# Kernel optimization log

Hardware: AMD Instinct MI355X
Metric: run time of the kernel (lower is better)

The kernel has to match this reference:

```python
import jax, jax.numpy as jnp
import numpy as np

LSTM_SIZE = 32
NUM_OPS = 64
NUM_EDGE = 128
TEMPERATURE = 5.0
TANH_CONST = 2.5


def _lstm_cell(x, h, c, W_ih, W_hh, b_ih, b_hh):
    # PyTorch gate order: i, f, g, o
    g = x @ W_ih.T + b_ih + h @ W_hh.T + b_hh  # [4*H]
    i, f, gg, o = jnp.split(g, 4)
    c2 = jax.nn.sigmoid(f) * c + jax.nn.sigmoid(i) * jnp.tanh(gg)
    h2 = jax.nn.sigmoid(o) * jnp.tanh(c2)
    return h2, c2


def setup_inputs() -> dict:
    key = jax.random.key(0)
    ks = jax.random.split(key, 12)
    H, G, O = LSTM_SIZE, 4 * LSTM_SIZE, NUM_OPS
    s = 0.1
    return {
        "input_vars": jax.random.uniform(ks[0], (1, 1, H), jnp.float32, -s, s),
        "W_ih0": jax.random.uniform(ks[1], (G, H), jnp.float32, -s, s),
        "W_hh0": jax.random.uniform(ks[2], (G, H), jnp.float32, -s, s),
        "b_ih0": jax.random.uniform(ks[3], (G,), jnp.float32, -s, s),
        "b_hh0": jax.random.uniform(ks[4], (G,), jnp.float32, -s, s),
        "W_ih1": jax.random.uniform(ks[5], (G, H), jnp.float32, -s, s),
        "W_hh1": jax.random.uniform(ks[6], (G, H), jnp.float32, -s, s),
        "b_ih1": jax.random.uniform(ks[7], (G,), jnp.float32, -s, s),
        "b_hh1": jax.random.uniform(ks[8], (G,), jnp.float32, -s, s),
        "embd": jax.random.uniform(ks[9], (O, H), jnp.float32, -s, s),
        "W_pred": jax.random.uniform(ks[10], (O, H), jnp.float32, -s, s),
        "b_pred": jax.random.uniform(ks[11], (O,), jnp.float32, -s, s),
        "num_edge": NUM_EDGE,
    }


def reference(input_vars, W_ih0, W_hh0, b_ih0, b_hh0,
              W_ih1, W_hh1, b_ih1, b_hh1,
              embd, W_pred, b_pred, num_edge):
    H = input_vars.shape[-1]
    x0 = input_vars.reshape(H)
    z = jnp.zeros((H,), input_vars.dtype)
    key0 = jax.random.key(42)

    def step(carry, _):
        key, x, h0, c0, h1, c1 = carry
        h0, c0 = _lstm_cell(x, h0, c0, W_ih0, W_hh0, b_ih0, b_hh0)
        h1, c1 = _lstm_cell(h0, h1, c1, W_ih1, W_hh1, b_ih1, b_hh1)
        logits = TANH_CONST * jnp.tanh((h1 @ W_pred.T + b_pred) / TEMPERATURE)
        key, sub = jax.random.split(key)
        idx = jax.random.categorical(sub, logits)
        logp = jax.nn.log_softmax(logits)
        lp = logp[idx]
        ent = -jnp.sum(jnp.exp(logp) * logp)
        x = embd[idx]
        return (key, x, h0, c0, h1, c1), (lp, ent, idx)

    _, (lps, ents, arch) = jax.lax.scan(step, (key0, x0, z, z, z, z), None, length=num_edge)
    return jnp.sum(lps), jnp.sum(ents), arch
```

## Files before the change

kernel.cpp:

```cpp
#include <hip/hip_runtime.h>
#include <stdint.h>

namespace {

typedef float v2f __attribute__((ext_vector_type(2)));
typedef int   v2i __attribute__((ext_vector_type(2)));

constexpr int H      = 32;
constexpr int NEDGE  = 128;
constexpr float TINY   = 1.1754943508222875e-38f;
constexpr float L2E    = 1.4426950408889634f;
constexpr float LN2    = 0.6931471805599453f;

__device__ __forceinline__ void tf_round(uint32_t& x0, uint32_t& x1, int r) {
  x0 += x1;
  x1 = (x1 << r) | (x1 >> (32 - r));
  x1 ^= x0;
}

__device__ __forceinline__ void tf2x32(uint32_t k0, uint32_t k1,
                                       uint32_t& x0, uint32_t& x1) {
  const uint32_t ks2 = k0 ^ k1 ^ 0x1BD11BDAu;
  x0 += k0; x1 += k1;
  tf_round(x0,x1,13); tf_round(x0,x1,15); tf_round(x0,x1,26); tf_round(x0,x1, 6);
  x0 += k1;  x1 += ks2 + 1u;
  tf_round(x0,x1,17); tf_round(x0,x1,29); tf_round(x0,x1,16); tf_round(x0,x1,24);
  x0 += ks2; x1 += k0 + 2u;
  tf_round(x0,x1,13); tf_round(x0,x1,15); tf_round(x0,x1,26); tf_round(x0,x1, 6);
  x0 += k0;  x1 += k1 + 3u;
  tf_round(x0,x1,17); tf_round(x0,x1,29); tf_round(x0,x1,16); tf_round(x0,x1,24);
  x0 += k1;  x1 += ks2 + 4u;
  tf_round(x0,x1,13); tf_round(x0,x1,15); tf_round(x0,x1,26); tf_round(x0,x1, 6);
  x0 += ks2; x1 += k0 + 5u;
}

__device__ __forceinline__ float fexp(float x) {
  return __builtin_amdgcn_exp2f(x * L2E);
}
__device__ __forceinline__ float flog(float x) {
  return __builtin_amdgcn_logf(x) * LN2;
}
__device__ __forceinline__ float fsigmoid(float x) {
  return __builtin_amdgcn_rcpf(1.0f + __builtin_amdgcn_exp2f(-x * L2E));
}
__device__ __forceinline__ float ftanh(float x) {
  const float ax = __builtin_fabsf(x);
  const float t  = __builtin_amdgcn_exp2f(ax * (-2.0f * L2E));
  const float r  = (1.0f - t) * __builtin_amdgcn_rcpf(1.0f + t);
  return __builtin_copysignf(r, x);
}

__device__ __forceinline__ float rdlane(float v, int i) {
  return __int_as_float(__builtin_amdgcn_readlane(__float_as_int(v), i));
}

template <int CTRL>
__device__ __forceinline__ float dppf(float v) {
  return __int_as_float(__builtin_amdgcn_update_dpp(
      __float_as_int(v), __float_as_int(v), CTRL, 0xF, 0xF, false));
}

__device__ __forceinline__ float wave_sum64(float v) {
  v += dppf<0xB1>(v);
  v += dppf<0x4E>(v);
  v += dppf<0x141>(v);
  v += dppf<0x140>(v);
  return (rdlane(v, 15) + rdlane(v, 31)) + (rdlane(v, 47) + rdlane(v, 63));
}

__device__ __forceinline__ float wave_max64(float v) {
  v = fmaxf(v, dppf<0xB1>(v));
  v = fmaxf(v, dppf<0x4E>(v));
  v = fmaxf(v, dppf<0x141>(v));
  v = fmaxf(v, dppf<0x140>(v));
  return fmaxf(fmaxf(rdlane(v, 15), rdlane(v, 31)),
               fmaxf(rdlane(v, 47), rdlane(v, 63)));
}

__device__ __forceinline__ v2f pkfma(v2f a, v2f b, v2f c) {
  return __builtin_elementwise_fma(a, b, c);
}

__device__ __forceinline__ v2f permswap_pair(float g) {
  const v2i r = __builtin_amdgcn_permlane32_swap(
      __float_as_int(g), __float_as_int(g), false, false);
  return v2f{__int_as_float(r.x), __int_as_float(r.y)};
}

__global__ __launch_bounds__(192, 1)
void ctrl_kernel(const float* __restrict__ input_vars,
                 const float* __restrict__ W_ih0, const float* __restrict__ W_hh0,
                 const float* __restrict__ b_ih0, const float* __restrict__ b_hh0,
                 const float* __restrict__ W_ih1, const float* __restrict__ W_hh1,
                 const float* __restrict__ b_ih1, const float* __restrict__ b_hh1,
                 const float* __restrict__ embd,
                 const float* __restrict__ W_pred, const float* __restrict__ b_pred,
                 float* __restrict__ out) {
  const int tid  = threadIdx.x;
  const int lane = tid & 63;
  const int wid  = tid >> 6;
  const int rB   = lane + 64;

  __shared__ float4 Wh[2][8][128];
  __shared__ __align__(16) float embd_lds[64 * H];
  __shared__ __align__(16) float h0buf[2][H];
  __shared__ __align__(16) float gumbuf[4][64];
  __shared__ __align__(16) float xbuf[2][H];
  __shared__ __align__(16) float arch_lds[NEDGE];

  if (wid < 2) {
#define STAGE(MAT, SRC)                                                    \
  _Pragma("unroll")                                                        \
  for (int j = 0; j < 8; ++j) {                                            \
    const int i = tid + 128 * j;                                           \
    const int k4 = i & 7, row = i >> 3;                                    \
    Wh[MAT][k4][row] = reinterpret_cast<const float4*>(SRC)[row * 8 + k4]; \
  }
    STAGE(0, W_hh0)
    STAGE(1, W_hh1)
#undef STAGE
#pragma unroll
    for (int j = 0; j < 4; ++j)
      reinterpret_cast<float4*>(embd_lds)[tid + 128 * j] =
          reinterpret_cast<const float4*>(embd)[tid + 128 * j];
    if (tid < 8)
      reinterpret_cast<float4*>(&xbuf[0][0])[tid] =
          reinterpret_cast<const float4*>(input_vars)[tid];
  }

  const float* WX = (wid == 1) ? W_ih1 : W_ih0;
  float4 wxA[8], wxB[8];
#pragma unroll
  for (int q = 0; q < 8; ++q) {
    wxA[q] = reinterpret_cast<const float4*>(WX + lane * H)[q];
    wxB[q] = reinterpret_cast<const float4*>(WX + rB * H)[q];
  }
  const float bsum0A = b_ih0[lane] + b_hh0[lane];
  const float bsum0B = b_ih0[rB]   + b_hh0[rB];
  const float bsum1A = b_ih1[lane] + b_hh1[lane];
  const float bsum1B = b_ih1[rB]   + b_hh1[rB];
  const float bp = b_pred[lane];
  float4 wp4[8];
#pragma unroll
  for (int q = 0; q < 8; ++q)
    wp4[q] = reinterpret_cast<const float4*>(W_pred + lane * H)[q];

  float c0 = 0.f, h0v = 0.f;
  float c1 = 0.f, h1v = 0.f;
  v2f hoA01={0.f,0.f}, hoA23={0.f,0.f}, hoB01={0.f,0.f}, hoB23={0.f,0.f};
  uint32_t k0 = 0u, k1 = 42u;
  uint32_t s0c = 0u, s1c = 0u;
  float lp_sum = 0.f, ent_sum = 0.f;
  float logit_prev = 0.f;
  int   idx_prev = 0;

  if (wid == 2) {
#pragma unroll 1
    for (int p = 0; p < 2; ++p) {
      uint32_t r0 = 0u, r1 = (uint32_t)(lane & 1);
      tf2x32(k0, k1, r0, r1);
      const uint32_t n0 = (uint32_t)__builtin_amdgcn_readlane((int)r0, 0);
      const uint32_t n1 = (uint32_t)__builtin_amdgcn_readlane((int)r1, 0);
      const uint32_t s0 = (uint32_t)__builtin_amdgcn_readlane((int)r0, 1);
      const uint32_t s1 = (uint32_t)__builtin_amdgcn_readlane((int)r1, 1);
      uint32_t x0 = 0u, x1 = (uint32_t)lane;
      tf2x32(s0, s1, x0, x1);
      const uint32_t bits = x0 ^ x1;
      k0 = n0; k1 = n1;
      float u = __uint_as_float(0x3f800000u | (bits >> 9)) - 1.0f;
      u = fmaxf(u + TINY, TINY);
      gumbuf[p][lane] = -flog(-flog(u));
    }
  }
  __syncthreads();

  for (int t = 0; t < NEDGE; ++t) {
    v2f rA01={0.f,0.f}, rA23={0.f,0.f}, rB01={0.f,0.f}, rB23={0.f,0.f};

    if (wid == 0) {
      v2f xA01={0.f,0.f}, xA23={0.f,0.f}, xB01={0.f,0.f}, xB23={0.f,0.f};
#pragma unroll
      for (int q = 0; q < 8; ++q) {
        const float4 x4 =
            *reinterpret_cast<const float4*>(&xbuf[t & 1][4 * q]);
        xA01 = pkfma(v2f{x4.x, x4.y}, v2f{wxA[q].x, wxA[q].y}, xA01);
        xA23 = pkfma(v2f{x4.z, x4.w}, v2f{wxA[q].z, wxA[q].w}, xA23);
        xB01 = pkfma(v2f{x4.x, x4.y}, v2f{wxB[q].x, wxB[q].y}, xB01);
        xB23 = pkfma(v2f{x4.z, x4.w}, v2f{wxB[q].z, wxB[q].w}, xB23);
      }
      const float gA = bsum0A + ((xA01.x + xA01.y) + (xA23.x + xA23.y))
                              + ((hoA01.x + hoA01.y) + (hoA23.x + hoA23.y));
      const float gB = bsum0B + ((xB01.x + xB01.y) + (xB23.x + xB23.y))
                              + ((hoB01.x + hoB01.y) + (hoB23.x + hoB23.y));
      const v2f gif = permswap_pair(gA);
      const v2f ggo = permswap_pair(gB);
      c0 = fsigmoid(gif.y) * c0 + fsigmoid(gif.x) * ftanh(ggo.x);
      h0v = fsigmoid(ggo.y) * ftanh(c0);
      h0buf[t & 1][lane & 31] = h0v;
    } else if (wid == 1) {
#pragma unroll
      for (int q = 0; q < 8; ++q) {
        const float4 wA = Wh[1][q][lane];
        const float4 wB = Wh[1][q][rB];
        const v2f h01 = {rdlane(h1v, 4*q+0), rdlane(h1v, 4*q+1)};
        const v2f h23 = {rdlane(h1v, 4*q+2), rdlane(h1v, 4*q+3)};
        rA01 = pkfma(h01, v2f{wA.x, wA.y}, rA01);
        rA23 = pkfma(h23, v2f{wA.z, wA.w}, rA23);
        rB01 = pkfma(h01, v2f{wB.x, wB.y}, rB01);
        rB23 = pkfma(h23, v2f{wB.z, wB.w}, rB23);
      }
      if (t > 0) {
        const float e  = fexp(logit_prev);
        const float E  = wave_sum64(e);
        const float ES = wave_sum64(e * logit_prev);
        const float lse = flog(E);
        const float li  = rdlane(logit_prev, idx_prev);
        lp_sum  += li - lse;
        ent_sum += lse - ES / E;
      }
    } else {
      uint32_t r0 = 0u, r1 = (uint32_t)(lane & 1);
      tf2x32(k0, k1, r0, r1);
      k0  = (uint32_t)__builtin_amdgcn_readlane((int)r0, 0);
      k1  = (uint32_t)__builtin_amdgcn_readlane((int)r1, 0);
      s0c = (uint32_t)__builtin_amdgcn_readlane((int)r0, 1);
      s1c = (uint32_t)__builtin_amdgcn_readlane((int)r1, 1);
    }
    __syncthreads();

    if (wid == 0) {
      hoA01 = v2f{0.f,0.f}; hoA23 = v2f{0.f,0.f};
      hoB01 = v2f{0.f,0.f}; hoB23 = v2f{0.f,0.f};
#pragma unroll
      for (int q = 0; q < 8; ++q) {
        const float4 wA = Wh[0][q][lane];
        const float4 wB = Wh[0][q][rB];
        const v2f h01 = {rdlane(h0v, 4*q+0), rdlane(h0v, 4*q+1)};
        const v2f h23 = {rdlane(h0v, 4*q+2), rdlane(h0v, 4*q+3)};
        hoA01 = pkfma(h01, v2f{wA.x, wA.y}, hoA01);
        hoA23 = pkfma(h23, v2f{wA.z, wA.w}, hoA23);
        hoB01 = pkfma(h01, v2f{wB.x, wB.y}, hoB01);
        hoB23 = pkfma(h23, v2f{wB.z, wB.w}, hoB23);
      }
    } else if (wid == 1) {
#pragma unroll
      for (int q = 0; q < 8; ++q) {
        const float4 h4 =
            *reinterpret_cast<const float4*>(&h0buf[t & 1][4 * q]);
        rA01 = pkfma(v2f{h4.x, h4.y}, v2f{wxA[q].x, wxA[q].y}, rA01);
        rA23 = pkfma(v2f{h4.z, h4.w}, v2f{wxA[q].z, wxA[q].w}, rA23);
        rB01 = pkfma(v2f{h4.x, h4.y}, v2f{wxB[q].x, wxB[q].y}, rB01);
        rB23 = pkfma(v2f{h4.z, h4.w}, v2f{wxB[q].z, wxB[q].w}, rB23);
      }
      const float gA1 = bsum1A + ((rA01.x + rA01.y) + (rA23.x + rA23.y));
      const float gB1 = bsum1B + ((rB01.x + rB01.y) + (rB23.x + rB23.y));
      const v2f gif1 = permswap_pair(gA1);
      const v2f ggo1 = permswap_pair(gB1);
      c1  = fsigmoid(gif1.y) * c1 + fsigmoid(gif1.x) * ftanh(ggo1.x);
      h1v = fsigmoid(ggo1.y) * ftanh(c1);

      v2f p01 = {0.f, 0.f}, p23 = {0.f, 0.f};
#pragma unroll
      for (int q = 0; q < 8; ++q) {
        const float4 w = wp4[q];
        p01 = pkfma(v2f{rdlane(h1v, 4*q+0), rdlane(h1v, 4*q+1)},
                    v2f{w.x, w.y}, p01);
        p23 = pkfma(v2f{rdlane(h1v, 4*q+2), rdlane(h1v, 4*q+3)},
                    v2f{w.z, w.w}, p23);
      }
      const float pre   = bp + ((p01.x + p01.y) + (p23.x + p23.y));
      const float logit = 2.5f * ftanh(pre * 0.2f);
      const float pert  = logit + gumbuf[t & 3][lane];

      const float M = wave_max64(pert);
      const unsigned long long msk = __ballot(pert == M);
      const int idxu = __ffsll((long long)msk) - 1;

      arch_lds[t] = (float)idxu;
      logit_prev = logit;
      idx_prev   = idxu;
      xbuf[(t + 1) & 1][lane & 31] = embd_lds[idxu * H + (lane & 31)];
    } else {
      uint32_t x0 = 0u, x1 = (uint32_t)lane;
      tf2x32(s0c, s1c, x0, x1);
      const uint32_t bits = x0 ^ x1;
      float u = __uint_as_float(0x3f800000u | (bits >> 9)) - 1.0f;
      u = fmaxf(u + TINY, TINY);
      gumbuf[(t + 2) & 3][lane] = -flog(-flog(u));
    }
    __syncthreads();
  }

  if (wid == 1) {
    const float e  = fexp(logit_prev);
    const float E  = wave_sum64(e);
    const float ES = wave_sum64(e * logit_prev);
    const float lse = flog(E);
    const float li  = rdlane(logit_prev, idx_prev);
    lp_sum  += li - lse;
    ent_sum += lse - ES / E;

    out[2 + lane]      = arch_lds[lane];
    out[2 + 64 + lane] = arch_lds[64 + lane];
    if (lane == 0) { out[0] = lp_sum; out[1] = ent_sum; }
  }
}

}

extern "C" void kernel_launch(void* const* d_in, const int* in_sizes, int n_in,
                              void* d_out, int out_size, void* d_ws, size_t ws_size,
                              hipStream_t stream) {
  (void)in_sizes; (void)n_in; (void)d_ws; (void)ws_size; (void)out_size;
  const float* input_vars = (const float*)d_in[0];
  const float* W_ih0 = (const float*)d_in[1];
  const float* W_hh0 = (const float*)d_in[2];
  const float* b_ih0 = (const float*)d_in[3];
  const float* b_hh0 = (const float*)d_in[4];
  const float* W_ih1 = (const float*)d_in[5];
  const float* W_hh1 = (const float*)d_in[6];
  const float* b_ih1 = (const float*)d_in[7];
  const float* b_hh1 = (const float*)d_in[8];
  const float* embd  = (const float*)d_in[9];
  const float* W_pred = (const float*)d_in[10];
  const float* b_pred = (const float*)d_in[11];
  float* out = (float*)d_out;

  hipLaunchKernelGGL(ctrl_kernel, dim3(1), dim3(192), 0, stream,
                     input_vars, W_ih0, W_hh0, b_ih0, b_hh0,
                     W_ih1, W_hh1, b_ih1, b_hh1,
                     embd, W_pred, b_pred, out);
}
```

Before: 136.8 us.

## Precompute embedding input projections and move logsumexp stats to RNG wave

Because layer-0 input is always one of 64 embedding rows (or the initial input), the kernel precomputes W_ih0·x for all 65 candidate inputs into an LDS table at startup. Each step then just gathers the selected row instead of doing a 32-wide dot product on the critical path. The log-softmax/entropy reduction moves from wave 1 to wave 2, which now reads logits and the chosen index through LDS. The startup cost rises with the 65x128 table build and extra LDS use (~33KB more), and the RNG key chain work is shifted into phase two.

```diff
diff --git a/kernel.cpp b/kernel.cpp
--- a/kernel.cpp
+++ b/kernel.cpp
@@ -102,57 +102,71 @@
   const int rB   = lane + 64;
 
   __shared__ float4 Wh[2][8][128];
-  __shared__ __align__(16) float embd_lds[64 * H];
+  __shared__ __align__(16) float embd_lds[65 * H];
+  __shared__ __align__(16) float xdot[65][128];
   __shared__ __align__(16) float h0buf[2][H];
   __shared__ __align__(16) float gumbuf[4][64];
-  __shared__ __align__(16) float xbuf[2][H];
+  __shared__ __align__(16) float xfer[2][2][64];
+  __shared__ __align__(16) float logitbuf[2][64];
   __shared__ __align__(16) float arch_lds[NEDGE];
 
-  if (wid < 2) {
 #define STAGE(MAT, SRC)                                                    \
   _Pragma("unroll")                                                        \
   for (int j = 0; j < 8; ++j) {                                            \
-    const int i = tid + 128 * j;                                           \
+    const int i = (tid & 127) + 128 * j;                                   \
     const int k4 = i & 7, row = i >> 3;                                    \
-    Wh[MAT][k4][row] = reinterpret_cast<const float4*>(SRC)[row * 8 + k4]; \
-  }
-    STAGE(0, W_hh0)
-    STAGE(1, W_hh1)
+    if (wid < 2)                                                           \
+      Wh[MAT][k4][row] = reinterpret_cast<const float4*>(SRC)[row * 8 + k4]; \
+  }
+  STAGE(0, W_hh0)
+  STAGE(1, W_hh1)
 #undef STAGE
-#pragma unroll
-    for (int j = 0; j < 4; ++j)
-      reinterpret_cast<float4*>(embd_lds)[tid + 128 * j] =
-          reinterpret_cast<const float4*>(embd)[tid + 128 * j];
-    if (tid < 8)
-      reinterpret_cast<float4*>(&xbuf[0][0])[tid] =
-          reinterpret_cast<const float4*>(input_vars)[tid];
-  }
-
-  const float* WX = (wid == 1) ? W_ih1 : W_ih0;
-  float4 wxA[8], wxB[8];
-#pragma unroll
-  for (int q = 0; q < 8; ++q) {
-    wxA[q] = reinterpret_cast<const float4*>(WX + lane * H)[q];
-    wxB[q] = reinterpret_cast<const float4*>(WX + rB * H)[q];
+  if (wid == 2) {
+#pragma unroll
+    for (int j = 0; j < 8; ++j)
+      reinterpret_cast<float4*>(embd_lds)[lane + 64 * j] =
+          reinterpret_cast<const float4*>(embd)[lane + 64 * j];
+    if (lane < 8)
+      reinterpret_cast<float4*>(&embd_lds[64 * H])[lane] =
+          reinterpret_cast<const float4*>(input_vars)[lane];
+  }
+  __syncthreads();
+
+  for (int e = tid; e < 65 * 128; e += 192) {
+    const int op = e >> 7, row = e & 127;
+    const float* xr = &embd_lds[op * H];
+    const float* wr = W_ih0 + row * H;
+    float c0 = 0.f, c1 = 0.f, c2 = 0.f, c3 = 0.f;
+#pragma unroll
+    for (int q = 0; q < 8; ++q) {
+      c0 = fmaf(xr[4*q+0], wr[4*q+0], c0);
+      c1 = fmaf(xr[4*q+1], wr[4*q+1], c1);
+      c2 = fmaf(xr[4*q+2], wr[4*q+2], c2);
+      c3 = fmaf(xr[4*q+3], wr[4*q+3], c3);
+    }
+    xdot[op][row] = (c0 + c1) + (c2 + c3);
+  }
+
+  float4 wxA[8], wxB[8], wp4[8];
+  if (wid == 1) {
+#pragma unroll
+    for (int q = 0; q < 8; ++q) {
+      wxA[q] = reinterpret_cast<const float4*>(W_ih1 + lane * H)[q];
+      wxB[q] = reinterpret_cast<const float4*>(W_ih1 + rB * H)[q];
+      wp4[q] = reinterpret_cast<const float4*>(W_pred + lane * H)[q];
+    }
   }
   const float bsum0A = b_ih0[lane] + b_hh0[lane];
   const float bsum0B = b_ih0[rB]   + b_hh0[rB];
   const float bsum1A = b_ih1[lane] + b_hh1[lane];
   const float bsum1B = b_ih1[rB]   + b_hh1[rB];
   const float bp = b_pred[lane];
-  float4 wp4[8];
-#pragma unroll
-  for (int q = 0; q < 8; ++q)
-    wp4[q] = reinterpret_cast<const float4*>(W_pred + lane * H)[q];
 
   float c0 = 0.f, h0v = 0.f;
   float c1 = 0.f, h1v = 0.f;
   v2f hoA01={0.f,0.f}, hoA23={0.f,0.f}, hoB01={0.f,0.f}, hoB23={0.f,0.f};
   uint32_t k0 = 0u, k1 = 42u;
-  uint32_t s0c = 0u, s1c = 0u;
   float lp_sum = 0.f, ent_sum = 0.f;
-  float logit_prev = 0.f;
-  int   idx_prev = 0;
 
   if (wid == 2) {
 #pragma unroll 1
@@ -174,24 +188,21 @@
   }
   __syncthreads();
 
+  if (wid == 0) {
+    xfer[0][0][lane] = xdot[64][lane];
+    xfer[0][1][lane] = xdot[64][rB];
+  }
+
   for (int t = 0; t < NEDGE; ++t) {
     v2f rA01={0.f,0.f}, rA23={0.f,0.f}, rB01={0.f,0.f}, rB23={0.f,0.f};
 
     if (wid == 0) {
-      v2f xA01={0.f,0.f}, xA23={0.f,0.f}, xB01={0.f,0.f}, xB23={0.f,0.f};
-#pragma unroll
-      for (int q = 0; q < 8; ++q) {
-        const float4 x4 =
-            *reinterpret_cast<const float4*>(&xbuf[t & 1][4 * q]);
-        xA01 = pkfma(v2f{x4.x, x4.y}, v2f{wxA[q].x, wxA[q].y}, xA01);
-        xA23 = pkfma(v2f{x4.z, x4.w}, v2f{wxA[q].z, wxA[q].w}, xA23);
-        xB01 = pkfma(v2f{x4.x, x4.y}, v2f{wxB[q].x, wxB[q].y}, xB01);
-        xB23 = pkfma(v2f{x4.z, x4.w}, v2f{wxB[q].z, wxB[q].w}, xB23);
-      }
-      const float gA = bsum0A + ((xA01.x + xA01.y) + (xA23.x + xA23.y))
-                              + ((hoA01.x + hoA01.y) + (hoA23.x + hoA23.y));
-      const float gB = bsum0B + ((xB01.x + xB01.y) + (xB23.x + xB23.y))
-                              + ((hoB01.x + hoB01.y) + (hoB23.x + hoB23.y));
+      const float xdA = xfer[t & 1][0][lane];
+      const float xdB = xfer[t & 1][1][lane];
+      const float gA = (bsum0A + xdA)
+                     + ((hoA01.x + hoA01.y) + (hoA23.x + hoA23.y));
+      const float gB = (bsum0B + xdB)
+                     + ((hoB01.x + hoB01.y) + (hoB23.x + hoB23.y));
       const v2f gif = permswap_pair(gA);
       const v2f ggo = permswap_pair(gB);
       c0 = fsigmoid(gif.y) * c0 + fsigmoid(gif.x) * ftanh(ggo.x);
@@ -209,22 +220,16 @@
         rB01 = pkfma(h01, v2f{wB.x, wB.y}, rB01);
         rB23 = pkfma(h23, v2f{wB.z, wB.w}, rB23);
       }
-      if (t > 0) {
-        const float e  = fexp(logit_prev);
-        const float E  = wave_sum64(e);
-        const float ES = wave_sum64(e * logit_prev);
-        const float lse = flog(E);
-        const float li  = rdlane(logit_prev, idx_prev);
-        lp_sum  += li - lse;
-        ent_sum += lse - ES / E;
-      }
-    } else {
-      uint32_t r0 = 0u, r1 = (uint32_t)(lane & 1);
-      tf2x32(k0, k1, r0, r1);
-      k0  = (uint32_t)__builtin_amdgcn_readlane((int)r0, 0);
-      k1  = (uint32_t)__builtin_amdgcn_readlane((int)r1, 0);
-      s0c = (uint32_t)__builtin_amdgcn_readlane((int)r0, 1);
-      s1c = (uint32_t)__builtin_amdgcn_readlane((int)r1, 1);
+    } else if (t > 0) {
+      const float lg  = logitbuf[(t - 1) & 1][lane];
+      const int  idxp = (int)arch_lds[t - 1];
+      const float e  = fexp(lg);
+      const float E  = wave_sum64(e);
+      const float ES = wave_sum64(e * lg);
+      const float lse = flog(E);
+      const float li  = logitbuf[(t - 1) & 1][idxp];
+      lp_sum  += li - lse;
+      ent_sum += lse - ES / E;
     }
     __syncthreads();
 
@@ -277,13 +282,20 @@
       const int idxu = __ffsll((long long)msk) - 1;
 
       arch_lds[t] = (float)idxu;
-      logit_prev = logit;
-      idx_prev   = idxu;
-      xbuf[(t + 1) & 1][lane & 31] = embd_lds[idxu * H + (lane & 31)];
+      logitbuf[t & 1][lane] = logit;
+      xfer[(t + 1) & 1][0][lane] = xdot[idxu][lane];
+      xfer[(t + 1) & 1][1][lane] = xdot[idxu][rB];
     } else {
+      uint32_t r0 = 0u, r1 = (uint32_t)(lane & 1);
+      tf2x32(k0, k1, r0, r1);
+      const uint32_t n0 = (uint32_t)__builtin_amdgcn_readlane((int)r0, 0);
+      const uint32_t n1 = (uint32_t)__builtin_amdgcn_readlane((int)r1, 0);
+      const uint32_t s0 = (uint32_t)__builtin_amdgcn_readlane((int)r0, 1);
+      const uint32_t s1 = (uint32_t)__builtin_amdgcn_readlane((int)r1, 1);
       uint32_t x0 = 0u, x1 = (uint32_t)lane;
-      tf2x32(s0c, s1c, x0, x1);
+      tf2x32(s0, s1, x0, x1);
       const uint32_t bits = x0 ^ x1;
+      k0 = n0; k1 = n1;
       float u = __uint_as_float(0x3f800000u | (bits >> 9)) - 1.0f;
       u = fmaxf(u + TINY, TINY);
       gumbuf[(t + 2) & 3][lane] = -flog(-flog(u));
@@ -291,18 +303,20 @@
     __syncthreads();
   }
 
-  if (wid == 1) {
-    const float e  = fexp(logit_prev);
+  if (wid == 2) {
+    const float lg  = logitbuf[127 & 1][lane];
+    const int  idxp = (int)arch_lds[127];
+    const float e  = fexp(lg);
     const float E  = wave_sum64(e);
-    const float ES = wave_sum64(e * logit_prev);
+    const float ES = wave_sum64(e * lg);
     const float lse = flog(E);
-    const float li  = rdlane(logit_prev, idx_prev);
+    const float li  = logitbuf[127 & 1][idxp];
     lp_sum  += li - lse;
     ent_sum += lse - ES / E;
-
+    if (lane == 0) { out[0] = lp_sum; out[1] = ent_sum; }
+  } else if (wid == 1) {
     out[2 + lane]      = arch_lds[lane];
     out[2 + 64 + lane] = arch_lds[64 + lane];
-    if (lane == 0) { out[0] = lp_sum; out[1] = ent_sum; }
   }
 }
 
```

Result: slower. 161.3 us (+17.9%).
